# Kernel tuning notes

Hardware: AMD Instinct MI355X
Metric: run time of the kernel (lower is better)

Reference implementation:

```python
import jax, jax.numpy as jnp
import numpy as np

N, C, W, H = 16, 64, 512, 512
RED, OUT_W = 64, 128
BN_EPS = 1e-5


def setup_inputs() -> dict:
    key = jax.random.key(0)
    ks = jax.random.split(key, 5)
    x = jax.random.normal(ks[0], (N, C, W, H), dtype=jnp.float32)
    w1 = jax.random.normal(ks[1], (RED, W), dtype=jnp.float32) * (1.0 / np.sqrt(W))
    b1 = jax.random.normal(ks[2], (RED,), dtype=jnp.float32) * 0.01
    gamma = jnp.ones((RED,), dtype=jnp.float32)
    beta = jnp.zeros((RED,), dtype=jnp.float32)
    w2 = jax.random.normal(ks[3], (W, RED), dtype=jnp.float32) * (1.0 / np.sqrt(RED))
    b2 = jax.random.normal(ks[4], (W,), dtype=jnp.float32) * 0.01
    return {"x": x, "w1": w1, "b1": b1, "gamma": gamma, "beta": beta, "w2": w2, "b2": b2}


def reference(x, w1, b1, gamma, beta, w2, b2):
    # attention_dim == 2: permute(0,2,1,3) -> [N,W,C,H]; AdaptiveMaxPool2d((1,1))
    # over (C,H) == global max over axes (1,3) of original x -> [N, W]
    pooled = jnp.max(x, axis=(1, 3))                       # [N, W]
    # Linear(W -> RED)
    h = pooled @ w1.T + b1                                 # [N, RED]
    # BatchNorm1d in training mode: batch stats (biased variance)
    mu = jnp.mean(h, axis=0)
    var = jnp.mean((h - mu) ** 2, axis=0)
    h = gamma * (h - mu) * jax.lax.rsqrt(var + BN_EPS) + beta
    h = jax.nn.relu(h)
    # Linear(RED -> W) + softmax over width
    att = jax.nn.softmax(h @ w2.T + b2, axis=1)            # [N, W]
    # topk over width, then sort selected indices ascending
    _, idx = jax.lax.top_k(att, OUT_W)                     # [N, OUT_W]
    idx = jnp.sort(idx, axis=1)
    # batched gather along width axis: x[i, :, idx[i], :]
    return jnp.take_along_axis(x, idx[:, None, :, None], axis=2)  # [N, C, OUT_W, H]
```

## Files before the change

### kernel.cpp

```cpp
#include <hip/hip_runtime.h>
#include <cstdint>
#include <math.h>

#define Nn   16
#define Cc   64
#define Ww   512
#define Hh   512
#define RED  64
#define OUTW 128

__global__ void __launch_bounds__(256) pool_kernel(const float* __restrict__ x,
                                                   float* __restrict__ pooled) {
    const int b = blockIdx.x;
    const int n = b >> 7;
    const int q = b & 127;
    const int r = threadIdx.x >> 6;
    const int lane = threadIdx.x & 63;
    const int w = q * 4 + r;
    const float* base = x + ((size_t)n * Cc * Ww + w) * Hh + lane * 8;
    const size_t cstride = (size_t)Ww * Hh;

    float m0 = -INFINITY, m1 = -INFINITY, m2 = -INFINITY, m3 = -INFINITY;
    float m4 = -INFINITY, m5 = -INFINITY, m6 = -INFINITY, m7 = -INFINITY;

    float4 a0 = *reinterpret_cast<const float4*>(base);
    float4 a1 = *reinterpret_cast<const float4*>(base + 4);
    float4 b0 = *reinterpret_cast<const float4*>(base + cstride);
    float4 b1 = *reinterpret_cast<const float4*>(base + cstride + 4);

    #pragma unroll 8
    for (int c = 0; c < Cc - 2; c += 2) {
        const float* p2 = base + (size_t)(c + 2) * cstride;
        const float* p3 = base + (size_t)(c + 3) * cstride;
        const float4 n0 = *reinterpret_cast<const float4*>(p2);
        const float4 n1 = *reinterpret_cast<const float4*>(p2 + 4);
        const float4 n2 = *reinterpret_cast<const float4*>(p3);
        const float4 n3 = *reinterpret_cast<const float4*>(p3 + 4);
        m0 = fmaxf(m0, a0.x); m1 = fmaxf(m1, a0.y);
        m2 = fmaxf(m2, a0.z); m3 = fmaxf(m3, a0.w);
        m4 = fmaxf(m4, a1.x); m5 = fmaxf(m5, a1.y);
        m6 = fmaxf(m6, a1.z); m7 = fmaxf(m7, a1.w);
        m0 = fmaxf(m0, b0.x); m1 = fmaxf(m1, b0.y);
        m2 = fmaxf(m2, b0.z); m3 = fmaxf(m3, b0.w);
        m4 = fmaxf(m4, b1.x); m5 = fmaxf(m5, b1.y);
        m6 = fmaxf(m6, b1.z); m7 = fmaxf(m7, b1.w);
        a0 = n0; a1 = n1; b0 = n2; b1 = n3;
    }
    m0 = fmaxf(m0, a0.x); m1 = fmaxf(m1, a0.y);
    m2 = fmaxf(m2, a0.z); m3 = fmaxf(m3, a0.w);
    m4 = fmaxf(m4, a1.x); m5 = fmaxf(m5, a1.y);
    m6 = fmaxf(m6, a1.z); m7 = fmaxf(m7, a1.w);
    m0 = fmaxf(m0, b0.x); m1 = fmaxf(m1, b0.y);
    m2 = fmaxf(m2, b0.z); m3 = fmaxf(m3, b0.w);
    m4 = fmaxf(m4, b1.x); m5 = fmaxf(m5, b1.y);
    m6 = fmaxf(m6, b1.z); m7 = fmaxf(m7, b1.w);

    float m = fmaxf(fmaxf(fmaxf(m0, m1), fmaxf(m2, m3)),
                    fmaxf(fmaxf(m4, m5), fmaxf(m6, m7)));
    #pragma unroll
    for (int off = 1; off < 64; off <<= 1)
        m = fmaxf(m, __shfl_xor(m, off, 64));
    if (lane == 0) pooled[n * Ww + w] = m;
}

__global__ void __launch_bounds__(256) mlp_h_kernel(
    const float* __restrict__ pooled,
    const float* __restrict__ w1,
    const float* __restrict__ b1,
    const float* __restrict__ gamma,
    const float* __restrict__ beta,
    float* __restrict__ hbn)
{
    const int r = blockIdx.x;
    const int t = threadIdx.x;
    const int n = t & 15;
    const int slice = t >> 4;
    const float4* w1r = reinterpret_cast<const float4*>(w1 + r * Ww + slice * 32);
    const float4* pn  = reinterpret_cast<const float4*>(pooled + n * Ww + slice * 32);

    float acc = 0.f;
    #pragma unroll
    for (int j = 0; j < 8; ++j) {
        const float4 a = w1r[j];
        const float4 p = pn[j];
        acc += a.x * p.x + a.y * p.y + a.z * p.z + a.w * p.w;
    }
    __shared__ float part[16][17];
    part[slice][n] = acc;
    __syncthreads();
    if (t < 16) {
        float h = b1[r];
        #pragma unroll
        for (int s = 0; s < 16; ++s) h += part[s][t];
        float sum = h, sq = h * h;
        #pragma unroll
        for (int off = 1; off < 16; off <<= 1) {
            sum += __shfl_xor(sum, off, 64);
            sq  += __shfl_xor(sq,  off, 64);
        }
        const float mu  = sum * (1.f / 16.f);
        const float var = sq  * (1.f / 16.f) - mu * mu;
        const float is  = 1.f / sqrtf(var + 1e-5f);
        const float v   = gamma[r] * (h - mu) * is + beta[r];
        hbn[r * Nn + t] = fmaxf(v, 0.f);
    }
}

__global__ void __launch_bounds__(512) logits_topk_kernel(
    const float* __restrict__ hbn,
    const float* __restrict__ w2,
    const float* __restrict__ b2,
    int* __restrict__ idx_out)
{
    const int row = blockIdx.x;
    const int w = threadIdx.x;

    __shared__ float hrow[RED];
    __shared__ float logits_row[Ww];
    __shared__ unsigned long long sel_mask[Ww / 64];

    float4 wv[16];
    const float4* w2r = reinterpret_cast<const float4*>(w2 + w * RED);
    #pragma unroll
    for (int j = 0; j < 16; ++j) wv[j] = w2r[j];
    if (w < RED) hrow[w] = hbn[w * Nn + row];
    __syncthreads();

    float acc = b2[w];
    #pragma unroll
    for (int j = 0; j < 16; ++j) {
        acc += wv[j].x * hrow[j * 4]     + wv[j].y * hrow[j * 4 + 1]
             + wv[j].z * hrow[j * 4 + 2] + wv[j].w * hrow[j * 4 + 3];
    }
    logits_row[w] = acc;
    __syncthreads();

    const float v = logits_row[w];
    int rank = 0;
    for (int ww = 0; ww < Ww; ++ww) {
        const float u = logits_row[ww];
        rank += (u > v || (u == v && ww < w)) ? 1 : 0;
    }
    const bool sel = (rank < OUTW);
    const unsigned long long m = __ballot(sel);
    if ((w & 63) == 0) sel_mask[w >> 6] = m;
    __syncthreads();
    if (sel) {
        int pos = 0;
        #pragma unroll
        for (int bb = 0; bb < (Ww / 64); ++bb)
            if (bb < (w >> 6)) pos += __popcll(sel_mask[bb]);
        pos += __popcll(sel_mask[w >> 6] & ((1ULL << (w & 63)) - 1ULL));
        idx_out[row * OUTW + pos] = w;
    }
}

__global__ void __launch_bounds__(256) gather_kernel(const float* __restrict__ x,
                                                     const int* __restrict__ idx,
                                                     float* __restrict__ out) {
    const int b = blockIdx.x;
    const int half = b & 1;
    const int nc = b >> 1;
    const int n = nc >> 6;
    const int tid = threadIdx.x;
    __shared__ int sidx[64];
    if (tid < 64) sidx[tid] = idx[n * OUTW + half * 64 + tid];
    __syncthreads();
    const float* src = x   + (size_t)nc * (Ww * Hh);
    float*       dst = out + (size_t)nc * (OUTW * Hh) + (size_t)half * 64 * Hh;
    #pragma unroll 8
    for (int i = tid; i < 64 * (Hh / 4); i += 256) {
        const int j = i >> 7;
        const int f = i & 127;
        const float4 v = *reinterpret_cast<const float4*>(src + (size_t)sidx[j] * Hh + f * 4);
        *reinterpret_cast<float4*>(dst + (size_t)j * Hh + f * 4) = v;
    }
}

extern "C" void kernel_launch(void* const* d_in, const int* in_sizes, int n_in,
                              void* d_out, int out_size, void* d_ws, size_t ws_size,
                              hipStream_t stream) {
    const float* x     = (const float*)d_in[0];
    const float* w1    = (const float*)d_in[1];
    const float* b1    = (const float*)d_in[2];
    const float* gamma = (const float*)d_in[3];
    const float* beta  = (const float*)d_in[4];
    const float* w2    = (const float*)d_in[5];
    const float* b2    = (const float*)d_in[6];
    float* out = (float*)d_out;

    float* pooled = (float*)d_ws;
    float* hbn    = (float*)((char*)d_ws + 32768);
    int*   idx    = (int*)((char*)d_ws + 32768 + 4096);

    pool_kernel<<<Nn * (Ww / 4), 256, 0, stream>>>(x, pooled);
    mlp_h_kernel<<<RED, 256, 0, stream>>>(pooled, w1, b1, gamma, beta, hbn);
    logits_topk_kernel<<<Nn, 512, 0, stream>>>(hbn, w2, b2, idx);
    gather_kernel<<<Nn * Cc * 2, 256, 0, stream>>>(x, idx, out);
}
```

Measured before the change: 318.6 us.

## Split max-pool into contiguous per-plane row max plus channel reduction

Replaces the strided pool kernel, which walked across channel planes with a stride of W*H per step, with a two-stage scheme. Each block streams half of one (n,c) plane contiguously and writes per-row maxima to a workspace buffer, and a small second kernel then reduces over channels. The aim is fully sequential, well-coalesced DRAM reads for the 1 GiB input. The cost is an extra launch and a 2 MiB intermediate buffer, and the new path runs only when the workspace is large enough, otherwise it falls back to the old kernel.

```diff
diff --git a/kernel.cpp b/kernel.cpp
--- a/kernel.cpp
+++ b/kernel.cpp
@@ -8,6 +8,58 @@
 #define Hh   512
 #define RED  64
 #define OUTW 128
+
+__global__ void __launch_bounds__(256) pool_contig_kernel(
+    const float* __restrict__ x, float* __restrict__ partial) {
+    const int b = blockIdx.x;
+    const int half = b & 1;
+    const int nc = b >> 1;
+    const float* plane = x + (size_t)nc * (Ww * Hh) + (size_t)half * 256 * Hh;
+    float* pout = partial + (size_t)nc * Ww + half * 256;
+    const int wv = threadIdx.x >> 6;
+    const int lane = threadIdx.x & 63;
+    const int g = lane >> 4;
+    const int s = lane & 15;
+
+    #pragma unroll 2
+    for (int step = 0; step < 16; ++step) {
+        const int rl = step * 16 + wv * 4 + g;
+        const float4* rp = reinterpret_cast<const float4*>(plane + (size_t)rl * Hh) + s;
+        const float4 v0 = rp[0];
+        const float4 v1 = rp[16];
+        const float4 v2 = rp[32];
+        const float4 v3 = rp[48];
+        const float4 v4 = rp[64];
+        const float4 v5 = rp[80];
+        const float4 v6 = rp[96];
+        const float4 v7 = rp[112];
+        float m = fmaxf(
+            fmaxf(fmaxf(fmaxf(fmaxf(v0.x, v0.y), fmaxf(v0.z, v0.w)),
+                        fmaxf(fmaxf(v1.x, v1.y), fmaxf(v1.z, v1.w))),
+                  fmaxf(fmaxf(fmaxf(v2.x, v2.y), fmaxf(v2.z, v2.w)),
+                        fmaxf(fmaxf(v3.x, v3.y), fmaxf(v3.z, v3.w)))),
+            fmaxf(fmaxf(fmaxf(fmaxf(v4.x, v4.y), fmaxf(v4.z, v4.w)),
+                        fmaxf(fmaxf(v5.x, v5.y), fmaxf(v5.z, v5.w))),
+                  fmaxf(fmaxf(fmaxf(v6.x, v6.y), fmaxf(v6.z, v6.w)),
+                        fmaxf(fmaxf(v7.x, v7.y), fmaxf(v7.z, v7.w)))));
+        m = fmaxf(m, __shfl_xor(m, 1, 64));
+        m = fmaxf(m, __shfl_xor(m, 2, 64));
+        m = fmaxf(m, __shfl_xor(m, 4, 64));
+        m = fmaxf(m, __shfl_xor(m, 8, 64));
+        if (s == 0) pout[rl] = m;
+    }
+}
+
+__global__ void __launch_bounds__(256) reduce_c_kernel(
+    const float* __restrict__ partial, float* __restrict__ pooled) {
+    const int o = blockIdx.x * 256 + threadIdx.x;
+    const int n = o >> 9, w = o & 511;
+    float m = -INFINITY;
+    #pragma unroll 8
+    for (int c = 0; c < Cc; ++c)
+        m = fmaxf(m, partial[((size_t)(n * Cc + c)) * Ww + w]);
+    pooled[o] = m;
+}
 
 __global__ void __launch_bounds__(256) pool_kernel(const float* __restrict__ x,
                                                    float* __restrict__ pooled) {
@@ -22,7 +74,6 @@
 
     float m0 = -INFINITY, m1 = -INFINITY, m2 = -INFINITY, m3 = -INFINITY;
     float m4 = -INFINITY, m5 = -INFINITY, m6 = -INFINITY, m7 = -INFINITY;
-
     float4 a0 = *reinterpret_cast<const float4*>(base);
     float4 a1 = *reinterpret_cast<const float4*>(base + 4);
     float4 b0 = *reinterpret_cast<const float4*>(base + cstride);
@@ -192,8 +243,15 @@
     float* pooled = (float*)d_ws;
     float* hbn    = (float*)((char*)d_ws + 32768);
     int*   idx    = (int*)((char*)d_ws + 32768 + 4096);
-
-    pool_kernel<<<Nn * (Ww / 4), 256, 0, stream>>>(x, pooled);
+    float* partial= (float*)((char*)d_ws + 65536);
+
+    const size_t need = 65536 + (size_t)Nn * Cc * Ww * sizeof(float);
+    if (ws_size >= need) {
+        pool_contig_kernel<<<Nn * Cc * 2, 256, 0, stream>>>(x, partial);
+        reduce_c_kernel<<<(Nn * Ww) / 256, 256, 0, stream>>>(partial, pooled);
+    } else {
+        pool_kernel<<<Nn * (Ww / 4), 256, 0, stream>>>(x, pooled);
+    }
     mlp_h_kernel<<<RED, 256, 0, stream>>>(pooled, w1, b1, gamma, beta, hbn);
     logits_topk_kernel<<<Nn, 512, 0, stream>>>(hbn, w2, b2, idx);
     gather_kernel<<<Nn * Cc * 2, 256, 0, stream>>>(x, idx, out);
```

Measured after the change: 349.9 us. 1.1x slower.
